# Optimization experiments

Measured on AMD Instinct MI355X. Metric: run time of the kernel, lower is better.

## Reference

```python
import jax, jax.numpy as jnp
import numpy as np


def _mlp(x, w1, b1, w2, b2):
    # x: [b,s,h]; w1: [h,f]; w2: [f,h]
    h = jax.nn.gelu(jnp.einsum('bsh,hf->bsf', x, w1) + b1, approximate=False)
    return jnp.einsum('bsf,fh->bsh', h, w2) + b2


def setup_inputs() -> dict:
    key = jax.random.key(0)
    ks = jax.random.split(key, 8)
    B, S, H, F, E, NS = 4, 1024, 1024, 2048, 8, 2
    sc_in = 1.0 / np.sqrt(H)
    sc_hid = 1.0 / np.sqrt(F)
    return {
        'x': jax.random.normal(ks[0], (B, S, H), jnp.float32),
        'shared_w1': jax.random.normal(ks[1], (NS, H, F), jnp.float32) * sc_in,
        'shared_b1': jnp.zeros((NS, F), jnp.float32),
        'shared_w2': jax.random.normal(ks[2], (NS, F, H), jnp.float32) * sc_hid,
        'shared_b2': jnp.zeros((NS, H), jnp.float32),
        'exp_w1': jax.random.normal(ks[3], (E, H, F), jnp.float32) * sc_in,
        'exp_b1': jnp.zeros((E, F), jnp.float32),
        'exp_w2': jax.random.normal(ks[4], (E, F, H), jnp.float32) * sc_hid,
        'exp_b2': jnp.zeros((E, H), jnp.float32),
        'router_w': jax.random.normal(ks[5], (H, E), jnp.float32) * sc_in,
        'router_b': jnp.zeros((E,), jnp.float32),
        'top_k': 2,
    }


def reference(x, shared_w1, shared_b1, shared_w2, shared_b2,
              exp_w1, exp_b1, exp_w2, exp_b2, router_w, router_b, top_k):
    E = exp_w1.shape[0]
    # shared experts: always active, summed
    share_out = jnp.zeros_like(x)
    for n in range(shared_w1.shape[0]):
        share_out = share_out + _mlp(x, shared_w1[n], shared_b1[n], shared_w2[n], shared_b2[n])

    # router: softmax + topk indices per token
    logits = jnp.einsum('bsh,he->bse', x, router_w) + router_b
    scores = jax.nn.softmax(logits, axis=-1)
    _, top_idx = jax.lax.top_k(scores, top_k)          # [b,s,k]
    mask = jax.nn.one_hot(top_idx, E, dtype=x.dtype).sum(axis=-2)  # [b,s,E]

    # routed experts: compute all, combine with top-k mask (unweighted, per source)
    hid = jax.nn.gelu(jnp.einsum('bsh,ehf->ebsf', x, exp_w1) + exp_b1[:, None, None, :],
                      approximate=False)
    exp_out = jnp.einsum('ebsf,efh->ebsh', hid, exp_w2) + exp_b2[:, None, None, :]
    routed = jnp.einsum('ebsh,bse->bsh', exp_out, mask)

    return share_out + routed
```

## Files before the change

### kernel.cpp

```cpp
#include <hip/hip_runtime.h>
#include <hip/hip_bf16.h>

#define T_TOK 4096
#define HD    1024
#define FD    2048
#define NEXP  8
#define NSH   2

using u16 = unsigned short;
typedef __bf16 bf16x8 __attribute__((ext_vector_type(8)));
typedef float  f32x4  __attribute__((ext_vector_type(4)));
typedef u16    u16x2  __attribute__((ext_vector_type(2)));
typedef u16    u16x4  __attribute__((ext_vector_type(4)));

__device__ __forceinline__ u16 f2bf(float f) {
    __hip_bfloat16 h = __float2bfloat16(f);
    u16 u; __builtin_memcpy(&u, &h, 2);
    return u;
}
__device__ __forceinline__ float bf2f(u16 u) {
    unsigned v = ((unsigned)u) << 16;
    float f; __builtin_memcpy(&f, &v, 4);
    return f;
}

__device__ __forceinline__ void gl2lds16(const u16* g, u16* l) {
    __builtin_amdgcn_global_load_lds((__attribute__((address_space(1))) void*)(g),
                                     (__attribute__((address_space(3))) void*)(l),
                                     16, 0, 0);
}

__device__ __forceinline__ void gemm_k_loop(
    const u16* a0, const u16* a1, const u16* b0, const u16* b1,
    u16* As, u16* Bs, int kIters, f32x4 acc[4][4])
{
    const int tid  = threadIdx.x;
    const int wave = tid >> 6, lane = tid & 63;
    const int wm = wave >> 1, wn = wave & 1;
    const int l16 = lane & 15, quad = lane >> 4;
    u16* lA0 = As + (wave * 32 + 0)  * 32 + lane * 8;
    u16* lA1 = As + (wave * 32 + 16) * 32 + lane * 8;
    u16* lB0 = Bs + (wave * 32 + 0)  * 32 + lane * 8;
    u16* lB1 = Bs + (wave * 32 + 16) * 32 + lane * 8;

    for (int kt = 0; kt < kIters; ++kt) {
        gl2lds16(a0, lA0);
        gl2lds16(a1, lA1);
        gl2lds16(b0, lB0);
        gl2lds16(b1, lB1);
        a0 += 32; a1 += 32; b0 += 32; b1 += 32;
        __syncthreads();
        bf16x8 af[4], bfv[4];
#pragma unroll
        for (int i = 0; i < 4; ++i)
            af[i] = *(const bf16x8*)(As + (wm * 64 + i * 16 + l16) * 32 + quad * 8);
#pragma unroll
        for (int j = 0; j < 4; ++j)
            bfv[j] = *(const bf16x8*)(Bs + (wn * 64 + j * 16 + l16) * 32 + quad * 8);
#pragma unroll
        for (int i = 0; i < 4; ++i)
#pragma unroll
            for (int j = 0; j < 4; ++j)
                acc[i][j] = __builtin_amdgcn_mfma_f32_16x16x32_bf16(af[i], bfv[j], acc[i][j], 0, 0, 0);
        __syncthreads();
    }
}

__device__ __forceinline__ float gelu_fast(float v) {
    float u = v * (0.7978845608028654f + 0.035677408136300125f * v * v);
    return v * __builtin_amdgcn_rcpf(1.0f + __expf(-2.0f * u));
}

#define EPI_STRIDE 68
template<bool GELU>
__device__ __forceinline__ void epi_store_bf16(
    f32x4 acc[4][4], const float bj[4],
    u16* __restrict__ dst, size_t ld, int rowbase, int colbase, u16* lds)
{
    const int lane = threadIdx.x & 63;
    const int l16 = lane & 15, quad = lane >> 4;
    const int rr = lane >> 2, seg = lane & 3;
#pragma unroll
    for (int i = 0; i < 4; ++i) {
#pragma unroll
        for (int j = 0; j < 4; ++j)
#pragma unroll
            for (int r = 0; r < 4; ++r) {
                float v = acc[i][j][r] + bj[j];
                if (GELU) v = gelu_fast(v);
                lds[(quad * 4 + r) * EPI_STRIDE + j * 16 + l16] = f2bf(v);
            }
        __asm__ volatile("s_waitcnt lgkmcnt(0)" ::: "memory");
        const u16* lp = lds + rr * EPI_STRIDE + seg * 16;
        u16x4 v0 = *(const u16x4*)(lp);
        u16x4 v1 = *(const u16x4*)(lp + 4);
        u16x4 v2 = *(const u16x4*)(lp + 8);
        u16x4 v3 = *(const u16x4*)(lp + 12);
        u16* gp = dst + (size_t)(rowbase + i * 16 + rr) * ld + colbase + seg * 16;
        *(u16x4*)(gp)      = v0;
        *(u16x4*)(gp + 4)  = v1;
        *(u16x4*)(gp + 8)  = v2;
        *(u16x4*)(gp + 12) = v3;
        __asm__ volatile("s_waitcnt lgkmcnt(0)" ::: "memory");
    }
}

__global__ __launch_bounds__(256) void router_convert_kernel(
    const float* __restrict__ x, const float* __restrict__ rw, const float* __restrict__ rb,
    u16* __restrict__ xb, int* __restrict__ cnt, int* __restrict__ lists, int* __restrict__ pos)
{
    const int t = blockIdx.x * 4 + (threadIdx.x >> 6);
    const int lane = threadIdx.x & 63;
    const float* xr = x + (size_t)t * HD;
    u16* xbr = xb + (size_t)t * HD;
    float acc[NEXP];
#pragma unroll
    for (int e = 0; e < NEXP; ++e) acc[e] = 0.f;
#pragma unroll
    for (int it = 0; it < 4; ++it) {
        int h0 = it * 256 + lane * 4;
        float4 v = *(const float4*)(xr + h0);
        ushort4 o = { f2bf(v.x), f2bf(v.y), f2bf(v.z), f2bf(v.w) };
        *(ushort4*)(xbr + h0) = o;
        float xv[4] = { v.x, v.y, v.z, v.w };
#pragma unroll
        for (int q = 0; q < 4; ++q) {
            const float4* wp = (const float4*)(rw + (size_t)(h0 + q) * NEXP);
            float4 w0 = wp[0], w1 = wp[1];
            acc[0] += xv[q] * w0.x; acc[1] += xv[q] * w0.y;
            acc[2] += xv[q] * w0.z; acc[3] += xv[q] * w0.w;
            acc[4] += xv[q] * w1.x; acc[5] += xv[q] * w1.y;
            acc[6] += xv[q] * w1.z; acc[7] += xv[q] * w1.w;
        }
    }
#pragma unroll
    for (int e = 0; e < NEXP; ++e)
        for (int off = 32; off; off >>= 1) acc[e] += __shfl_xor(acc[e], off, 64);
    if (lane == 0) {
#pragma unroll
        for (int e = 0; e < NEXP; ++e) acc[e] += rb[e];
        int b1i = 0;
        for (int e = 1; e < NEXP; ++e) if (acc[e] > acc[b1i]) b1i = e;
        int b2i = (b1i == 0) ? 1 : 0;
        for (int e = 0; e < NEXP; ++e) if (e != b1i && acc[e] > acc[b2i]) b2i = e;
        int p1 = atomicAdd(&cnt[b1i], 1); lists[b1i * T_TOK + p1] = t;
        int p2 = atomicAdd(&cnt[b2i], 1); lists[b2i * T_TOK + p2] = t;
        pos[2 * t]     = (b1i << 13) | p1;
        pos[2 * t + 1] = (b2i << 13) | p2;
    }
}

__global__ void offsets_kernel(const int* __restrict__ cnt, int* __restrict__ pfx) {
    if (threadIdx.x == 0 && blockIdx.x == 0) {
        int s = 0;
        for (int e = 0; e < NEXP; ++e) { pfx[e] = s; s += ((cnt[e] + 127) >> 7) << 7; }
        pfx[NEXP] = s;
    }
}

__global__ __launch_bounds__(256) void transpose_w1_kernel(
    const float* __restrict__ sw1, const float* __restrict__ ew1, u16* __restrict__ wt)
{
    __shared__ u16 tile[32][65];
    const int z = blockIdx.z;
    const float* src = (z < NSH) ? (sw1 + (size_t)z * HD * FD)
                                 : (ew1 + (size_t)(z - NSH) * HD * FD);
    u16* dst = wt + (size_t)z * FD * HD;
    const int tx = threadIdx.x, ty = threadIdx.y;
    const int c0 = blockIdx.x * 32;
    const int r0 = blockIdx.y * 64;
#pragma unroll
    for (int k = 0; k < 8; ++k)
        tile[tx][ty + 8 * k] = f2bf(src[(size_t)(r0 + ty + 8 * k) * FD + c0 + tx]);
    __syncthreads();
#pragma unroll
    for (int k = 0; k < 4; ++k) {
        int c = ty + 8 * k;
        u16x2 v = { tile[c][2 * tx], tile[c][2 * tx + 1] };
        *(u16x2*)(dst + (size_t)(c0 + c) * HD + r0 + 2 * tx) = v;
    }
}

__global__ __launch_bounds__(256) void transpose_w2_kernel(
    const float* __restrict__ sw2, const float* __restrict__ ew2, u16* __restrict__ wt)
{
    __shared__ u16 tile[32][65];
    const int z = blockIdx.z;
    const float* src; u16* dst; size_t ldd;
    if (z < NSH) { src = sw2 + (size_t)z * FD * HD; dst = wt + (size_t)z * FD; ldd = 2 * FD; }
    else { src = ew2 + (size_t)(z - NSH) * FD * HD;
           dst = wt + (size_t)NSH * FD * HD + (size_t)(z - NSH) * HD * FD; ldd = FD; }
    const int tx = threadIdx.x, ty = threadIdx.y;
    const int c0 = blockIdx.x * 32;
    const int r0 = blockIdx.y * 64;
#pragma unroll
    for (int k = 0; k < 8; ++k)
        tile[tx][ty + 8 * k] = f2bf(src[(size_t)(r0 + ty + 8 * k) * HD + c0 + tx]);
    __syncthreads();
#pragma unroll
    for (int k = 0; k < 4; ++k) {
        int c = ty + 8 * k;
        u16x2 v = { tile[c][2 * tx], tile[c][2 * tx + 1] };
        *(u16x2*)(dst + (size_t)(c0 + c) * ldd + r0 + 2 * tx) = v;
    }
}

__global__ __launch_bounds__(256, 4) void gemm1_all_kernel(
    const u16* __restrict__ xb, const u16* __restrict__ w1t,
    const float* __restrict__ sb1, const float* __restrict__ eb1,
    const int* __restrict__ cnt, const int* __restrict__ pfx,
    const int* __restrict__ lists,
    u16* __restrict__ hidS, u16* __restrict__ hidE)
{
    const int z = blockIdx.z, nt = blockIdx.x, mt = blockIdx.y;
    const bool routed = (z >= NSH);
    const int e = z - NSH;
    if (routed && mt * 128 >= cnt[e]) return;
    __shared__ __align__(16) u16 S[2 * 128 * 32];
    u16* As = S;
    u16* Bs = S + 128 * 32;
    const int tid = threadIdx.x, wave = tid >> 6, lane = tid & 63;
    const int r0 = wave * 32 + (lane >> 2), ch = (lane & 3) * 8;
    const u16 *a0, *a1;
    if (routed) {
        int tok0 = lists[e * T_TOK + mt * 128 + r0];
        int tok1 = lists[e * T_TOK + mt * 128 + r0 + 16];
        a0 = xb + (size_t)tok0 * HD + ch;
        a1 = xb + (size_t)tok1 * HD + ch;
    } else {
        a0 = xb + (size_t)(mt * 128 + r0) * HD + ch;
        a1 = a0 + (size_t)16 * HD;
    }
    const u16* b0 = w1t + (size_t)z * FD * HD + (size_t)(nt * 128 + r0) * HD + ch;
    const u16* b1 = b0 + (size_t)16 * HD;
    f32x4 acc[4][4] = {};
    gemm_k_loop(a0, a1, b0, b1, As, Bs, HD / 32, acc);

    const int wm = wave >> 1, wn = wave & 1, l16 = lane & 15;
    const float* bias = routed ? (eb1 + e * FD) : (sb1 + z * FD);
    float bj[4];
#pragma unroll
    for (int j = 0; j < 4; ++j) bj[j] = bias[nt * 128 + wn * 64 + j * 16 + l16];
    u16* dst   = routed ? hidE : hidS;
    const size_t ld = routed ? FD : 2 * FD;
    const int rowbase = (routed ? (pfx[e] + mt * 128) : (mt * 128)) + wm * 64;
    const int colbase = (routed ? 0 : z * FD) + nt * 128 + wn * 64;
    epi_store_bf16<true>(acc, bj, dst, ld, rowbase, colbase, S + wave * 16 * EPI_STRIDE);
}

__global__ __launch_bounds__(256, 4) void gemm2_all_kernel(
    const u16* __restrict__ hidS, const u16* __restrict__ hidE,
    const u16* __restrict__ w2t,
    const float* __restrict__ sb2, const float* __restrict__ eb2,
    const int* __restrict__ cnt, const int* __restrict__ pfx,
    float* __restrict__ out, u16* __restrict__ routedOut)
{
    const int z = blockIdx.z, nt = blockIdx.x, mt = blockIdx.y;
    const int e = z - 1;
    if (z >= 1 && mt * 128 >= cnt[e]) return;
    __shared__ __align__(16) u16 S[2 * 128 * 32];
    u16* As = S;
    u16* Bs = S + 128 * 32;
    const int tid = threadIdx.x, wave = tid >> 6, lane = tid & 63;
    const int r0 = wave * 32 + (lane >> 2), ch = (lane & 3) * 8;
    const int wm = wave >> 1, wn = wave & 1, l16 = lane & 15, quad = lane >> 4;
    f32x4 acc[4][4] = {};

    if (z == 0) {
        const u16* a0 = hidS + (size_t)(mt * 128 + r0) * (2 * FD) + ch;
        const u16* a1 = a0 + (size_t)16 * (2 * FD);
        const u16* b0 = w2t + (size_t)(nt * 128 + r0) * (2 * FD) + ch;
        const u16* b1 = b0 + (size_t)16 * (2 * FD);
        gemm_k_loop(a0, a1, b0, b1, As, Bs, (2 * FD) / 32, acc);
#pragma unroll
        for (int j = 0; j < 4; ++j) {
            int h = nt * 128 + wn * 64 + j * 16 + l16;
            float bv = sb2[h] + sb2[HD + h];
#pragma unroll
            for (int i = 0; i < 4; ++i) {
                int row = mt * 128 + wm * 64 + i * 16 + quad * 4;
#pragma unroll
                for (int r = 0; r < 4; ++r)
                    out[(size_t)(row + r) * HD + h] = acc[i][j][r] + bv;
            }
        }
    } else {
        const int base = pfx[e];
        const u16* a0 = hidE + (size_t)(base + mt * 128 + r0) * FD + ch;
        const u16* a1 = a0 + (size_t)16 * FD;
        const u16* b0 = w2t + (size_t)NSH * FD * HD + (size_t)e * HD * FD
                            + (size_t)(nt * 128 + r0) * FD + ch;
        const u16* b1 = b0 + (size_t)16 * FD;
        gemm_k_loop(a0, a1, b0, b1, As, Bs, FD / 32, acc);
        float bj[4];
#pragma unroll
        for (int j = 0; j < 4; ++j) bj[j] = eb2[e * HD + nt * 128 + wn * 64 + j * 16 + l16];
        epi_store_bf16<false>(acc, bj, routedOut, HD,
                              base + mt * 128 + wm * 64, nt * 128 + wn * 64,
                              S + wave * 16 * EPI_STRIDE);
    }
}

__global__ __launch_bounds__(256, 4) void gemm2_routed_atomic_kernel(
    const u16* __restrict__ hidE, const u16* __restrict__ w2t,
    const float* __restrict__ eb2, const int* __restrict__ cnt,
    const int* __restrict__ pfx, const int* __restrict__ lists,
    float* __restrict__ out)
{
    const int e = blockIdx.z, nt = blockIdx.x, mt = blockIdx.y;
    const int n_e = cnt[e];
    if (mt * 128 >= n_e) return;
    __shared__ __align__(16) u16 S[2 * 128 * 32];
    u16* As = S;
    u16* Bs = S + 128 * 32;
    const int tid = threadIdx.x, wave = tid >> 6, lane = tid & 63;
    const int r0 = wave * 32 + (lane >> 2), ch = (lane & 3) * 8;
    const int base = pfx[e];
    const u16* a0 = hidE + (size_t)(base + mt * 128 + r0) * FD + ch;
    const u16* a1 = a0 + (size_t)16 * FD;
    const u16* b0 = w2t + (size_t)NSH * FD * HD + (size_t)e * HD * FD
                        + (size_t)(nt * 128 + r0) * FD + ch;
    const u16* b1 = b0 + (size_t)16 * FD;
    f32x4 acc[4][4] = {};
    gemm_k_loop(a0, a1, b0, b1, As, Bs, FD / 32, acc);
    const int wm = wave >> 1, wn = wave & 1, l16 = lane & 15, quad = lane >> 4;
#pragma unroll
    for (int j = 0; j < 4; ++j) {
        int h = nt * 128 + wn * 64 + j * 16 + l16;
        float bv = eb2[e * HD + h];
#pragma unroll
        for (int i = 0; i < 4; ++i) {
            int local = mt * 128 + wm * 64 + i * 16 + quad * 4;
#pragma unroll
            for (int r = 0; r < 4; ++r)
                if (local + r < n_e) {
                    int t = lists[e * T_TOK + local + r];
                    atomicAdd(&out[(size_t)t * HD + h], acc[i][j][r] + bv);
                }
        }
    }
}

__global__ __launch_bounds__(256) void finalize_kernel(
    const u16* __restrict__ routedOut, const int* __restrict__ pos,
    const int* __restrict__ pfx, float* __restrict__ out)
{
    const int t = blockIdx.x;
    int enc0 = pos[2 * t], enc1 = pos[2 * t + 1];
    int row0 = pfx[enc0 >> 13] + (enc0 & 8191);
    int row1 = pfx[enc1 >> 13] + (enc1 & 8191);
    int h = threadIdx.x * 4;
    ushort4 a = *(const ushort4*)(routedOut + (size_t)row0 * HD + h);
    ushort4 b = *(const ushort4*)(routedOut + (size_t)row1 * HD + h);
    float* po = out + (size_t)t * HD + h;
    float4 o = *(const float4*)po;
    o.x += bf2f(a.x) + bf2f(b.x);
    o.y += bf2f(a.y) + bf2f(b.y);
    o.z += bf2f(a.z) + bf2f(b.z);
    o.w += bf2f(a.w) + bf2f(b.w);
    *(float4*)po = o;
}

extern "C" void kernel_launch(void* const* d_in, const int* in_sizes, int n_in,
                              void* d_out, int out_size, void* d_ws, size_t ws_size,
                              hipStream_t stream)
{
    (void)in_sizes; (void)n_in; (void)out_size;
    const float* x   = (const float*)d_in[0];
    const float* sw1 = (const float*)d_in[1];
    const float* sb1 = (const float*)d_in[2];
    const float* sw2 = (const float*)d_in[3];
    const float* sb2 = (const float*)d_in[4];
    const float* ew1 = (const float*)d_in[5];
    const float* eb1 = (const float*)d_in[6];
    const float* ew2 = (const float*)d_in[7];
    const float* eb2 = (const float*)d_in[8];
    const float* rw  = (const float*)d_in[9];
    const float* rb  = (const float*)d_in[10];
    float* out = (float*)d_out;

    const bool plain = (ws_size >= (size_t)132284544);
    char* ws   = (char*)d_ws;
    u16*  wt   = (u16*)ws;
    u16*  hidS = (u16*)(ws + 41943040);
    u16*  hidE = (u16*)(ws + 75497472);
    u16*  xb   = (u16*)(ws + 113246208);
    u16*  rOut = (u16*)(ws + 113246208);
    size_t smallOfs = plain ? (size_t)132120576 : (size_t)121634816;
    int*  cnt   = (int*)(ws + smallOfs);
    int*  pfx   = (int*)(ws + smallOfs + 64);
    int*  lists = (int*)(ws + smallOfs + 128);
    int*  pos   = (int*)(ws + smallOfs + 128 + NEXP * T_TOK * 4);

    hipMemsetAsync(cnt, 0, 128 + (size_t)NEXP * T_TOK * 4, stream);

    router_convert_kernel<<<dim3(T_TOK / 4), dim3(256), 0, stream>>>(x, rw, rb, xb, cnt, lists, pos);
    offsets_kernel<<<dim3(1), dim3(64), 0, stream>>>(cnt, pfx);
    transpose_w1_kernel<<<dim3(FD / 32, HD / 64, NSH + NEXP), dim3(32, 8), 0, stream>>>(sw1, ew1, wt);

    gemm1_all_kernel<<<dim3(FD / 128, T_TOK / 128, NSH + NEXP), dim3(256), 0, stream>>>(
        xb, wt, sb1, eb1, cnt, pfx, lists, hidS, hidE);

    transpose_w2_kernel<<<dim3(HD / 32, FD / 64, NSH + NEXP), dim3(32, 8), 0, stream>>>(sw2, ew2, wt);

    if (plain) {
        gemm2_all_kernel<<<dim3(HD / 128, T_TOK / 128, 1 + NEXP), dim3(256), 0, stream>>>(
            hidS, hidE, wt, sb2, eb2, cnt, pfx, out, rOut);
        finalize_kernel<<<dim3(T_TOK), dim3(256), 0, stream>>>(rOut, pos, pfx, out);
    } else {
        gemm2_all_kernel<<<dim3(HD / 128, T_TOK / 128, 1), dim3(256), 0, stream>>>(
            hidS, hidE, wt, sb2, eb2, cnt, pfx, out, rOut);
        gemm2_routed_atomic_kernel<<<dim3(HD / 128, T_TOK / 128, NEXP), dim3(256), 0, stream>>>(
            hidE, wt, eb2, cnt, pfx, lists, out);
    }
}
```

Before: 523.4 us.

## Rewrite expert GEMMs with 256x256 tiles, pipelined LDS staging, split-K atomic output

Replaces the 128x128, 32-deep K loop with a 512-thread 256x256 tile core. It uses 64-wide K tiles, double-buffered LDS with an XOR swizzle, staged async loads interleaved with MFMA phases, and priority hints. It adds an XCD-aware block remap and splits the second GEMM's K in half per shared and routed expert. Results go through fp32 atomics into a zeroed output, which removes the bf16 routed scratch buffer and the finalize pass. The cost is more atomic traffic and an extra memset, plus nondeterministic summation order.

```diff
diff --git a/kernel.cpp b/kernel.cpp
--- a/kernel.cpp
+++ b/kernel.cpp
@@ -18,11 +18,6 @@
     u16 u; __builtin_memcpy(&u, &h, 2);
     return u;
 }
-__device__ __forceinline__ float bf2f(u16 u) {
-    unsigned v = ((unsigned)u) << 16;
-    float f; __builtin_memcpy(&f, &v, 4);
-    return f;
-}
 
 __device__ __forceinline__ void gl2lds16(const u16* g, u16* l) {
     __builtin_amdgcn_global_load_lds((__attribute__((address_space(1))) void*)(g),
@@ -30,58 +25,116 @@
                                      16, 0, 0);
 }
 
-__device__ __forceinline__ void gemm_k_loop(
-    const u16* a0, const u16* a1, const u16* b0, const u16* b1,
-    u16* As, u16* Bs, int kIters, f32x4 acc[4][4])
-{
-    const int tid  = threadIdx.x;
-    const int wave = tid >> 6, lane = tid & 63;
-    const int wm = wave >> 1, wn = wave & 1;
-    const int l16 = lane & 15, quad = lane >> 4;
-    u16* lA0 = As + (wave * 32 + 0)  * 32 + lane * 8;
-    u16* lA1 = As + (wave * 32 + 16) * 32 + lane * 8;
-    u16* lB0 = Bs + (wave * 32 + 0)  * 32 + lane * 8;
-    u16* lB1 = Bs + (wave * 32 + 16) * 32 + lane * 8;
-
-    for (int kt = 0; kt < kIters; ++kt) {
-        gl2lds16(a0, lA0);
-        gl2lds16(a1, lA1);
-        gl2lds16(b0, lB0);
-        gl2lds16(b1, lB1);
-        a0 += 32; a1 += 32; b0 += 32; b1 += 32;
-        __syncthreads();
-        bf16x8 af[4], bfv[4];
-#pragma unroll
-        for (int i = 0; i < 4; ++i)
-            af[i] = *(const bf16x8*)(As + (wm * 64 + i * 16 + l16) * 32 + quad * 8);
-#pragma unroll
-        for (int j = 0; j < 4; ++j)
-            bfv[j] = *(const bf16x8*)(Bs + (wn * 64 + j * 16 + l16) * 32 + quad * 8);
-#pragma unroll
-        for (int i = 0; i < 4; ++i)
-#pragma unroll
-            for (int j = 0; j < 4; ++j)
-                acc[i][j] = __builtin_amdgcn_mfma_f32_16x16x32_bf16(af[i], bfv[j], acc[i][j], 0, 0, 0);
-        __syncthreads();
-    }
-}
-
 __device__ __forceinline__ float gelu_fast(float v) {
     float u = v * (0.7978845608028654f + 0.035677408136300125f * v * v);
     return v * __builtin_amdgcn_rcpf(1.0f + __expf(-2.0f * u));
 }
 
+template<int Q>
+__device__ __forceinline__ void stage_q(const u16* const rb[8], u16* S,
+                                        int bufsel, int ktile, int nT) {
+    if (ktile >= nT) return;
+    constexpr int isB = Q >> 1, half = Q & 1;
+    u16* dst = S + (bufsel * 2 + isB) * 16384 + half * 8192 + threadIdx.x * 8;
+    constexpr int base = isB * 4 + half * 2;
+    gl2lds16(rb[base + 0] + (size_t)ktile * 64, dst);
+    gl2lds16(rb[base + 1] + (size_t)ktile * 64, dst + 4096);
+}
+
+__device__ __forceinline__ void core256(const u16* const rb[8], u16* S,
+                                        int nT, f32x4 acc[8][4]) {
+    const int tid = threadIdx.x, wave = tid >> 6, lane = tid & 63;
+    const int wm = wave >> 2, wn = wave & 3;
+    const int l16 = lane & 15, quad = lane >> 4;
+    const int xr = l16 >> 1;
+    stage_q<0>(rb, S, 0, 0, nT); stage_q<1>(rb, S, 0, 0, nT);
+    stage_q<2>(rb, S, 0, 0, nT); stage_q<3>(rb, S, 0, 0, nT);
+    stage_q<0>(rb, S, 1, 1, nT); stage_q<1>(rb, S, 1, 1, nT);
+    asm volatile("s_waitcnt vmcnt(4)" ::: "memory");
+    __builtin_amdgcn_s_barrier();
+    __builtin_amdgcn_sched_barrier(0);
+    for (int t = 0; t < nT; ++t) {
+        const int cur = t & 1;
+        const u16* At = S + cur * 32768;
+        const u16* Bt = At + 16384;
+        const u16* Arow = At + (wm * 128 + l16) * 64;
+        const u16* Brow = Bt + (wn * 64 + l16) * 64;
+        bf16x8 a0[8], b0[4], a1[8], b1[4];
+#pragma unroll
+        for (int i = 0; i < 8; ++i)
+            a0[i] = *(const bf16x8*)(Arow + i * 1024 + ((quad ^ xr) * 8));
+#pragma unroll
+        for (int j = 0; j < 4; ++j)
+            b0[j] = *(const bf16x8*)(Brow + j * 1024 + ((quad ^ xr) * 8));
+        stage_q<2>(rb, S, cur ^ 1, t + 1, nT);
+        __builtin_amdgcn_s_barrier();
+        asm volatile("s_waitcnt lgkmcnt(0)" ::: "memory");
+        __builtin_amdgcn_sched_barrier(0);
+        __builtin_amdgcn_s_setprio(1);
+#pragma unroll
+        for (int i = 0; i < 4; ++i)
+#pragma unroll
+            for (int j = 0; j < 4; ++j)
+                acc[i][j] = __builtin_amdgcn_mfma_f32_16x16x32_bf16(a0[i], b0[j], acc[i][j], 0, 0, 0);
+        __builtin_amdgcn_s_setprio(0);
+        __builtin_amdgcn_s_barrier();
+#pragma unroll
+        for (int i = 0; i < 8; ++i)
+            a1[i] = *(const bf16x8*)(Arow + i * 1024 + (((4 + quad) ^ xr) * 8));
+        stage_q<3>(rb, S, cur ^ 1, t + 1, nT);
+        __builtin_amdgcn_s_barrier();
+        asm volatile("s_waitcnt lgkmcnt(0)" ::: "memory");
+        __builtin_amdgcn_sched_barrier(0);
+        __builtin_amdgcn_s_setprio(1);
+#pragma unroll
+        for (int i = 0; i < 4; ++i)
+#pragma unroll
+            for (int j = 0; j < 4; ++j)
+                acc[4 + i][j] = __builtin_amdgcn_mfma_f32_16x16x32_bf16(a0[4 + i], b0[j], acc[4 + i][j], 0, 0, 0);
+        __builtin_amdgcn_s_setprio(0);
+        __builtin_amdgcn_s_barrier();
+#pragma unroll
+        for (int j = 0; j < 4; ++j)
+            b1[j] = *(const bf16x8*)(Brow + j * 1024 + (((4 + quad) ^ xr) * 8));
+        stage_q<0>(rb, S, cur, t + 2, nT);
+        __builtin_amdgcn_s_barrier();
+        asm volatile("s_waitcnt lgkmcnt(0)" ::: "memory");
+        __builtin_amdgcn_sched_barrier(0);
+        __builtin_amdgcn_s_setprio(1);
+#pragma unroll
+        for (int i = 0; i < 4; ++i)
+#pragma unroll
+            for (int j = 0; j < 4; ++j)
+                acc[i][j] = __builtin_amdgcn_mfma_f32_16x16x32_bf16(a1[i], b1[j], acc[i][j], 0, 0, 0);
+        __builtin_amdgcn_s_setprio(0);
+        __builtin_amdgcn_s_barrier();
+        stage_q<1>(rb, S, cur, t + 2, nT);
+        __builtin_amdgcn_s_barrier();
+        __builtin_amdgcn_s_setprio(1);
+#pragma unroll
+        for (int i = 0; i < 4; ++i)
+#pragma unroll
+            for (int j = 0; j < 4; ++j)
+                acc[4 + i][j] = __builtin_amdgcn_mfma_f32_16x16x32_bf16(a1[4 + i], b1[j], acc[4 + i][j], 0, 0, 0);
+        __builtin_amdgcn_s_setprio(0);
+        if (t < nT - 2)       asm volatile("s_waitcnt vmcnt(4)" ::: "memory");
+        else if (t == nT - 2) asm volatile("s_waitcnt vmcnt(0)" ::: "memory");
+        __builtin_amdgcn_s_barrier();
+        __builtin_amdgcn_sched_barrier(0);
+    }
+}
+
 #define EPI_STRIDE 68
 template<bool GELU>
-__device__ __forceinline__ void epi_store_bf16(
-    f32x4 acc[4][4], const float bj[4],
-    u16* __restrict__ dst, size_t ld, int rowbase, int colbase, u16* lds)
+__device__ __forceinline__ void epi_bf16_w(
+    f32x4 acc[8][4], const float bj[4],
+    u16* __restrict__ dst, size_t ld, int row0, int colbase, int rowmax, u16* lds)
 {
     const int lane = threadIdx.x & 63;
     const int l16 = lane & 15, quad = lane >> 4;
     const int rr = lane >> 2, seg = lane & 3;
 #pragma unroll
-    for (int i = 0; i < 4; ++i) {
+    for (int i = 0; i < 8; ++i) {
 #pragma unroll
         for (int j = 0; j < 4; ++j)
 #pragma unroll
@@ -90,24 +143,37 @@
                 if (GELU) v = gelu_fast(v);
                 lds[(quad * 4 + r) * EPI_STRIDE + j * 16 + l16] = f2bf(v);
             }
-        __asm__ volatile("s_waitcnt lgkmcnt(0)" ::: "memory");
-        const u16* lp = lds + rr * EPI_STRIDE + seg * 16;
-        u16x4 v0 = *(const u16x4*)(lp);
-        u16x4 v1 = *(const u16x4*)(lp + 4);
-        u16x4 v2 = *(const u16x4*)(lp + 8);
-        u16x4 v3 = *(const u16x4*)(lp + 12);
-        u16* gp = dst + (size_t)(rowbase + i * 16 + rr) * ld + colbase + seg * 16;
-        *(u16x4*)(gp)      = v0;
-        *(u16x4*)(gp + 4)  = v1;
-        *(u16x4*)(gp + 8)  = v2;
-        *(u16x4*)(gp + 12) = v3;
-        __asm__ volatile("s_waitcnt lgkmcnt(0)" ::: "memory");
-    }
+        asm volatile("s_waitcnt lgkmcnt(0)" ::: "memory");
+        const int grow = row0 + i * 16 + rr;
+        if (grow < rowmax) {
+            const u16* lp = lds + rr * EPI_STRIDE + seg * 16;
+            u16x4 v0 = *(const u16x4*)(lp);
+            u16x4 v1 = *(const u16x4*)(lp + 4);
+            u16x4 v2 = *(const u16x4*)(lp + 8);
+            u16x4 v3 = *(const u16x4*)(lp + 12);
+            u16* gp = dst + (size_t)grow * ld + colbase + seg * 16;
+            *(u16x4*)(gp)      = v0;
+            *(u16x4*)(gp + 4)  = v1;
+            *(u16x4*)(gp + 8)  = v2;
+            *(u16x4*)(gp + 12) = v3;
+        }
+        asm volatile("s_waitcnt lgkmcnt(0)" ::: "memory");
+    }
+}
+
+template<int NX, int NWG>
+__device__ __forceinline__ void xcd_map(int z, int& nt, int& mt) {
+    const int flat = blockIdx.x + NX * blockIdx.y;
+    constexpr int q = NWG >> 3;
+    const int xcd = (flat - z) & 7;
+    const int s = xcd * q + (flat >> 3);
+    nt = s % NX;
+    mt = s / NX;
 }
 
 __global__ __launch_bounds__(256) void router_convert_kernel(
     const float* __restrict__ x, const float* __restrict__ rw, const float* __restrict__ rb,
-    u16* __restrict__ xb, int* __restrict__ cnt, int* __restrict__ lists, int* __restrict__ pos)
+    u16* __restrict__ xb, int* __restrict__ cnt, int* __restrict__ lists)
 {
     const int t = blockIdx.x * 4 + (threadIdx.x >> 6);
     const int lane = threadIdx.x & 63;
@@ -145,8 +211,6 @@
         for (int e = 0; e < NEXP; ++e) if (e != b1i && acc[e] > acc[b2i]) b2i = e;
         int p1 = atomicAdd(&cnt[b1i], 1); lists[b1i * T_TOK + p1] = t;
         int p2 = atomicAdd(&cnt[b2i], 1); lists[b2i * T_TOK + p2] = t;
-        pos[2 * t]     = (b1i << 13) | p1;
-        pos[2 * t + 1] = (b2i << 13) | p2;
     }
 }
 
@@ -205,167 +269,145 @@
     }
 }
 
-__global__ __launch_bounds__(256, 4) void gemm1_all_kernel(
+__global__ __launch_bounds__(512, 2) void gemm1_all_256(
     const u16* __restrict__ xb, const u16* __restrict__ w1t,
     const float* __restrict__ sb1, const float* __restrict__ eb1,
     const int* __restrict__ cnt, const int* __restrict__ pfx,
     const int* __restrict__ lists,
     u16* __restrict__ hidS, u16* __restrict__ hidE)
 {
-    const int z = blockIdx.z, nt = blockIdx.x, mt = blockIdx.y;
+    const int z = blockIdx.z;
+    int nt, mt; xcd_map<FD / 256, (FD / 256) * (T_TOK / 256)>(z, nt, mt);
     const bool routed = (z >= NSH);
     const int e = z - NSH;
-    if (routed && mt * 128 >= cnt[e]) return;
-    __shared__ __align__(16) u16 S[2 * 128 * 32];
-    u16* As = S;
-    u16* Bs = S + 128 * 32;
-    const int tid = threadIdx.x, wave = tid >> 6, lane = tid & 63;
-    const int r0 = wave * 32 + (lane >> 2), ch = (lane & 3) * 8;
-    const u16 *a0, *a1;
+    int ce = 0, pe = 0;
+    if (routed) { ce = cnt[e]; pe = pfx[e]; if (mt * 256 >= ce) return; }
+    __shared__ __align__(16) u16 S[4 * 16384];
+    const int tid = threadIdx.x;
+    const int u = tid >> 3;
+    const int cl = (tid & 7) ^ ((tid >> 4) & 7);
+    const u16* rb[8];
     if (routed) {
-        int tok0 = lists[e * T_TOK + mt * 128 + r0];
-        int tok1 = lists[e * T_TOK + mt * 128 + r0 + 16];
-        a0 = xb + (size_t)tok0 * HD + ch;
-        a1 = xb + (size_t)tok1 * HD + ch;
+#pragma unroll
+        for (int q = 0; q < 4; ++q) {
+            const int tok = lists[e * T_TOK + mt * 256 + q * 64 + u];
+            rb[q] = xb + (size_t)tok * HD + cl * 8;
+        }
     } else {
-        a0 = xb + (size_t)(mt * 128 + r0) * HD + ch;
-        a1 = a0 + (size_t)16 * HD;
-    }
-    const u16* b0 = w1t + (size_t)z * FD * HD + (size_t)(nt * 128 + r0) * HD + ch;
-    const u16* b1 = b0 + (size_t)16 * HD;
-    f32x4 acc[4][4] = {};
-    gemm_k_loop(a0, a1, b0, b1, As, Bs, HD / 32, acc);
-
-    const int wm = wave >> 1, wn = wave & 1, l16 = lane & 15;
+#pragma unroll
+        for (int q = 0; q < 4; ++q)
+            rb[q] = xb + (size_t)(mt * 256 + q * 64 + u) * HD + cl * 8;
+    }
+    const u16* wb = w1t + (size_t)z * FD * HD + (size_t)(nt * 256 + u) * HD + cl * 8;
+#pragma unroll
+    for (int q = 0; q < 4; ++q) rb[4 + q] = wb + (size_t)(q * 64) * HD;
+
+    f32x4 acc[8][4] = {};
+    core256(rb, S, HD / 64, acc);
+
+    const int wave = tid >> 6, lane = tid & 63;
+    const int wm = wave >> 2, wn = wave & 3, l16 = lane & 15;
     const float* bias = routed ? (eb1 + e * FD) : (sb1 + z * FD);
     float bj[4];
 #pragma unroll
-    for (int j = 0; j < 4; ++j) bj[j] = bias[nt * 128 + wn * 64 + j * 16 + l16];
-    u16* dst   = routed ? hidE : hidS;
+    for (int j = 0; j < 4; ++j) bj[j] = bias[nt * 256 + wn * 64 + j * 16 + l16];
+    u16* dst = routed ? hidE : hidS;
     const size_t ld = routed ? FD : 2 * FD;
-    const int rowbase = (routed ? (pfx[e] + mt * 128) : (mt * 128)) + wm * 64;
-    const int colbase = (routed ? 0 : z * FD) + nt * 128 + wn * 64;
-    epi_store_bf16<true>(acc, bj, dst, ld, rowbase, colbase, S + wave * 16 * EPI_STRIDE);
-}
-
-__global__ __launch_bounds__(256, 4) void gemm2_all_kernel(
+    const int colbase = (routed ? 0 : z * FD) + nt * 256 + wn * 64;
+    const int row0 = (routed ? pe : 0) + mt * 256 + wm * 128;
+    const int rowmax = routed ? (pe + ((ce + 127) & ~127)) : (1 << 30);
+    epi_bf16_w<true>(acc, bj, dst, ld, row0, colbase, rowmax, S + wave * 16 * EPI_STRIDE);
+}
+
+__global__ __launch_bounds__(512, 2) void gemm2_all_256(
     const u16* __restrict__ hidS, const u16* __restrict__ hidE,
     const u16* __restrict__ w2t,
     const float* __restrict__ sb2, const float* __restrict__ eb2,
     const int* __restrict__ cnt, const int* __restrict__ pfx,
-    float* __restrict__ out, u16* __restrict__ routedOut)
-{
-    const int z = blockIdx.z, nt = blockIdx.x, mt = blockIdx.y;
-    const int e = z - 1;
-    if (z >= 1 && mt * 128 >= cnt[e]) return;
-    __shared__ __align__(16) u16 S[2 * 128 * 32];
-    u16* As = S;
-    u16* Bs = S + 128 * 32;
-    const int tid = threadIdx.x, wave = tid >> 6, lane = tid & 63;
-    const int r0 = wave * 32 + (lane >> 2), ch = (lane & 3) * 8;
-    const int wm = wave >> 1, wn = wave & 1, l16 = lane & 15, quad = lane >> 4;
-    f32x4 acc[4][4] = {};
-
-    if (z == 0) {
-        const u16* a0 = hidS + (size_t)(mt * 128 + r0) * (2 * FD) + ch;
-        const u16* a1 = a0 + (size_t)16 * (2 * FD);
-        const u16* b0 = w2t + (size_t)(nt * 128 + r0) * (2 * FD) + ch;
-        const u16* b1 = b0 + (size_t)16 * (2 * FD);
-        gemm_k_loop(a0, a1, b0, b1, As, Bs, (2 * FD) / 32, acc);
-#pragma unroll
-        for (int j = 0; j < 4; ++j) {
-            int h = nt * 128 + wn * 64 + j * 16 + l16;
-            float bv = sb2[h] + sb2[HD + h];
-#pragma unroll
-            for (int i = 0; i < 4; ++i) {
-                int row = mt * 128 + wm * 64 + i * 16 + quad * 4;
-#pragma unroll
-                for (int r = 0; r < 4; ++r)
-                    out[(size_t)(row + r) * HD + h] = acc[i][j][r] + bv;
+    const int* __restrict__ lists,
+    float* __restrict__ out)
+{
+    const int z = blockIdx.z;
+    int nt, mt; xcd_map<HD / 256, (HD / 256) * (T_TOK / 256)>(z, nt, mt);
+    const bool sharedp = (z < 2 * NSH);
+    const int e = (z - 2 * NSH) >> 1;
+    const int kh = sharedp ? (z & 1) : ((z - 2 * NSH) & 1);
+    int ce = 0, pe = 0;
+    if (!sharedp) { ce = cnt[e]; pe = pfx[e]; if (mt * 256 >= ce) return; }
+    __shared__ __align__(16) u16 S[4 * 16384];
+    const int tid = threadIdx.x;
+    const int u = tid >> 3;
+    const int cl = (tid & 7) ^ ((tid >> 4) & 7);
+    const u16* rb[8];
+    if (sharedp) {
+        const int s = z >> 1;
+        const u16* ab = hidS + (size_t)s * FD + (size_t)kh * (FD / 2) + cl * 8;
+        const u16* bb = w2t + (size_t)s * FD + (size_t)kh * (FD / 2) + cl * 8;
+#pragma unroll
+        for (int q = 0; q < 4; ++q) {
+            rb[q]     = ab + (size_t)(mt * 256 + q * 64 + u) * (2 * FD);
+            rb[4 + q] = bb + (size_t)(nt * 256 + q * 64 + u) * (2 * FD);
+        }
+    } else {
+        const u16* ab = hidE + (size_t)(pe + mt * 256 + u) * FD + (size_t)kh * (FD / 2) + cl * 8;
+        const u16* bb = w2t + (size_t)NSH * FD * HD + (size_t)e * HD * FD
+                      + (size_t)(nt * 256 + u) * FD + (size_t)kh * (FD / 2) + cl * 8;
+#pragma unroll
+        for (int q = 0; q < 4; ++q) {
+            rb[q]     = ab + (size_t)(q * 64) * FD;
+            rb[4 + q] = bb + (size_t)(q * 64) * FD;
+        }
+    }
+    f32x4 acc[8][4] = {};
+    core256(rb, S, (FD / 2) / 64, acc);
+
+    const int wave = tid >> 6, lane = tid & 63;
+    const int wm = wave >> 2, wn = wave & 3, l16 = lane & 15, quad = lane >> 4;
+    float bj[4];
+#pragma unroll
+    for (int j = 0; j < 4; ++j) {
+        const int h = nt * 256 + wn * 64 + j * 16 + l16;
+        float bv = 0.0f;
+        if (sharedp) { if (z == 0) bv = sb2[h] + sb2[HD + h]; }
+        else if (kh == 0) bv = eb2[e * HD + h];
+        bj[j] = bv;
+    }
+    const int cb = nt * 256 + wn * 64 + l16;
+    if (sharedp) {
+#pragma unroll
+        for (int i = 0; i < 8; ++i) {
+            const int row = mt * 256 + wm * 128 + i * 16 + quad * 4;
+#pragma unroll
+            for (int r = 0; r < 4; ++r) {
+                float* po = out + (size_t)(row + r) * HD + cb;
+#pragma unroll
+                for (int j = 0; j < 4; ++j)
+                    atomicAdd(po + j * 16, acc[i][j][r] + bj[j]);
             }
         }
     } else {
-        const int base = pfx[e];
-        const u16* a0 = hidE + (size_t)(base + mt * 128 + r0) * FD + ch;
-        const u16* a1 = a0 + (size_t)16 * FD;
-        const u16* b0 = w2t + (size_t)NSH * FD * HD + (size_t)e * HD * FD
-                            + (size_t)(nt * 128 + r0) * FD + ch;
-        const u16* b1 = b0 + (size_t)16 * FD;
-        gemm_k_loop(a0, a1, b0, b1, As, Bs, FD / 32, acc);
-        float bj[4];
-#pragma unroll
-        for (int j = 0; j < 4; ++j) bj[j] = eb2[e * HD + nt * 128 + wn * 64 + j * 16 + l16];
-        epi_store_bf16<false>(acc, bj, routedOut, HD,
-                              base + mt * 128 + wm * 64, nt * 128 + wn * 64,
-                              S + wave * 16 * EPI_STRIDE);
-    }
-}
-
-__global__ __launch_bounds__(256, 4) void gemm2_routed_atomic_kernel(
-    const u16* __restrict__ hidE, const u16* __restrict__ w2t,
-    const float* __restrict__ eb2, const int* __restrict__ cnt,
-    const int* __restrict__ pfx, const int* __restrict__ lists,
-    float* __restrict__ out)
-{
-    const int e = blockIdx.z, nt = blockIdx.x, mt = blockIdx.y;
-    const int n_e = cnt[e];
-    if (mt * 128 >= n_e) return;
-    __shared__ __align__(16) u16 S[2 * 128 * 32];
-    u16* As = S;
-    u16* Bs = S + 128 * 32;
-    const int tid = threadIdx.x, wave = tid >> 6, lane = tid & 63;
-    const int r0 = wave * 32 + (lane >> 2), ch = (lane & 3) * 8;
-    const int base = pfx[e];
-    const u16* a0 = hidE + (size_t)(base + mt * 128 + r0) * FD + ch;
-    const u16* a1 = a0 + (size_t)16 * FD;
-    const u16* b0 = w2t + (size_t)NSH * FD * HD + (size_t)e * HD * FD
-                        + (size_t)(nt * 128 + r0) * FD + ch;
-    const u16* b1 = b0 + (size_t)16 * FD;
-    f32x4 acc[4][4] = {};
-    gemm_k_loop(a0, a1, b0, b1, As, Bs, FD / 32, acc);
-    const int wm = wave >> 1, wn = wave & 1, l16 = lane & 15, quad = lane >> 4;
-#pragma unroll
-    for (int j = 0; j < 4; ++j) {
-        int h = nt * 128 + wn * 64 + j * 16 + l16;
-        float bv = eb2[e * HD + h];
-#pragma unroll
-        for (int i = 0; i < 4; ++i) {
-            int local = mt * 128 + wm * 64 + i * 16 + quad * 4;
-#pragma unroll
-            for (int r = 0; r < 4; ++r)
-                if (local + r < n_e) {
-                    int t = lists[e * T_TOK + local + r];
-                    atomicAdd(&out[(size_t)t * HD + h], acc[i][j][r] + bv);
+#pragma unroll
+        for (int i = 0; i < 8; ++i) {
+            const int rloc = mt * 256 + wm * 128 + i * 16 + quad * 4;
+#pragma unroll
+            for (int r = 0; r < 4; ++r) {
+                if (rloc + r < ce) {
+                    const int tok = lists[e * T_TOK + rloc + r];
+                    float* po = out + (size_t)tok * HD + cb;
+#pragma unroll
+                    for (int j = 0; j < 4; ++j)
+                        atomicAdd(po + j * 16, acc[i][j][r] + bj[j]);
                 }
-        }
-    }
-}
-
-__global__ __launch_bounds__(256) void finalize_kernel(
-    const u16* __restrict__ routedOut, const int* __restrict__ pos,
-    const int* __restrict__ pfx, float* __restrict__ out)
-{
-    const int t = blockIdx.x;
-    int enc0 = pos[2 * t], enc1 = pos[2 * t + 1];
-    int row0 = pfx[enc0 >> 13] + (enc0 & 8191);
-    int row1 = pfx[enc1 >> 13] + (enc1 & 8191);
-    int h = threadIdx.x * 4;
-    ushort4 a = *(const ushort4*)(routedOut + (size_t)row0 * HD + h);
-    ushort4 b = *(const ushort4*)(routedOut + (size_t)row1 * HD + h);
-    float* po = out + (size_t)t * HD + h;
-    float4 o = *(const float4*)po;
-    o.x += bf2f(a.x) + bf2f(b.x);
-    o.y += bf2f(a.y) + bf2f(b.y);
-    o.z += bf2f(a.z) + bf2f(b.z);
-    o.w += bf2f(a.w) + bf2f(b.w);
-    *(float4*)po = o;
+            }
+        }
+    }
 }
 
 extern "C" void kernel_launch(void* const* d_in, const int* in_sizes, int n_in,
                               void* d_out, int out_size, void* d_ws, size_t ws_size,
                               hipStream_t stream)
 {
-    (void)in_sizes; (void)n_in; (void)out_size;
+    (void)in_sizes; (void)n_in; (void)out_size; (void)ws_size;
     const float* x   = (const float*)d_in[0];
     const float* sw1 = (const float*)d_in[1];
     const float* sb1 = (const float*)d_in[2];
@@ -379,38 +421,27 @@
     const float* rb  = (const float*)d_in[10];
     float* out = (float*)d_out;
 
-    const bool plain = (ws_size >= (size_t)132284544);
     char* ws   = (char*)d_ws;
     u16*  wt   = (u16*)ws;
     u16*  hidS = (u16*)(ws + 41943040);
     u16*  hidE = (u16*)(ws + 75497472);
     u16*  xb   = (u16*)(ws + 113246208);
-    u16*  rOut = (u16*)(ws + 113246208);
-    size_t smallOfs = plain ? (size_t)132120576 : (size_t)121634816;
-    int*  cnt   = (int*)(ws + smallOfs);
-    int*  pfx   = (int*)(ws + smallOfs + 64);
-    int*  lists = (int*)(ws + smallOfs + 128);
-    int*  pos   = (int*)(ws + smallOfs + 128 + NEXP * T_TOK * 4);
+    int*  cnt   = (int*)(ws + 121634816);
+    int*  pfx   = (int*)(ws + 121634816 + 64);
+    int*  lists = (int*)(ws + 121634816 + 128);
 
     hipMemsetAsync(cnt, 0, 128 + (size_t)NEXP * T_TOK * 4, stream);
-
-    router_convert_kernel<<<dim3(T_TOK / 4), dim3(256), 0, stream>>>(x, rw, rb, xb, cnt, lists, pos);
+    hipMemsetAsync(out, 0, (size_t)T_TOK * HD * 4, stream);
+
+    router_convert_kernel<<<dim3(T_TOK / 4), dim3(256), 0, stream>>>(x, rw, rb, xb, cnt, lists);
     offsets_kernel<<<dim3(1), dim3(64), 0, stream>>>(cnt, pfx);
     transpose_w1_kernel<<<dim3(FD / 32, HD / 64, NSH + NEXP), dim3(32, 8), 0, stream>>>(sw1, ew1, wt);
 
-    gemm1_all_kernel<<<dim3(FD / 128, T_TOK / 128, NSH + NEXP), dim3(256), 0, stream>>>(
+    gemm1_all_256<<<dim3(FD / 256, T_TOK / 256, NSH + NEXP), dim3(512), 0, stream>>>(
         xb, wt, sb1, eb1, cnt, pfx, lists, hidS, hidE);
 
     transpose_w2_kernel<<<dim3(HD / 32, FD / 64, NSH + NEXP), dim3(32, 8), 0, stream>>>(sw2, ew2, wt);
 
-    if (plain) {
-        gemm2_all_kernel<<<dim3(HD / 128, T_TOK / 128, 1 + NEXP), dim3(256), 0, stream>>>(
-            hidS, hidE, wt, sb2, eb2, cnt, pfx, out, rOut);
-        finalize_kernel<<<dim3(T_TOK), dim3(256), 0, stream>>>(rOut, pos, pfx, out);
-    } else {
-        gemm2_all_kernel<<<dim3(HD / 128, T_TOK / 128, 1), dim3(256), 0, stream>>>(
-            hidS, hidE, wt, sb2, eb2, cnt, pfx, out, rOut);
-        gemm2_routed_atomic_kernel<<<dim3(HD / 128, T_TOK / 128, NEXP), dim3(256), 0, stream>>>(
-            hidE, wt, eb2, cnt, pfx, lists, out);
-    }
-}
+    gemm2_all_256<<<dim3(HD / 256, T_TOK / 256, 2 * NSH + 2 * NEXP), dim3(512), 0, stream>>>(
+        hidS, hidE, wt, sb2, eb2, cnt, pfx, lists, out);
+}
```

Measured after the change: 587.2 us. +12.2%, slower.
